# Optimization experiments

Hardware: AMD Instinct MI355X
Metric: run time of the kernel (lower is better)

Reference implementation:

```python
import jax, jax.numpy as jnp
import numpy as np

NEG_SLOPE = 0.2


def gat_layer(x, W, a_src, a_dst, b, src, dst, n_nodes):
    """Single-head GATConv (PyG defaults: heads=1, concat, leaky_relu 0.2, bias)."""
    h = x @ W                                  # [N, hid]
    e_src = h @ a_src                          # [N] per-source logits
    e_dst = h @ a_dst                          # [N] per-dest logits
    e = jax.nn.leaky_relu(e_src[src] + e_dst[dst], NEG_SLOPE)  # [E]
    # numerically-stable softmax over variable-degree dst neighborhoods
    m = jax.ops.segment_max(e, dst, num_segments=n_nodes)
    ex = jnp.exp(e - m[dst])
    s = jax.ops.segment_sum(ex, dst, num_segments=n_nodes)
    alpha = ex / s[dst]                        # [E]
    out = jax.ops.segment_sum(alpha[:, None] * h[src], dst, num_segments=n_nodes)
    return out + b


def setup_inputs() -> dict:
    key = jax.random.key(0)
    N, E, F_IN, HID = 100000, 3200000, 128, 64
    ks = jax.random.split(key, 16)
    x = jax.random.normal(ks[0], (N, F_IN), dtype=jnp.float32)
    edge_index = jax.random.randint(ks[1], (2, E), 0, N, dtype=jnp.int64)
    d = {"x": x, "edge_index": edge_index}
    dims = [(F_IN, HID), (HID, HID), (HID, HID)]
    for i, (din, dout) in enumerate(dims, start=1):
        sc = 1.0 / np.sqrt(din)
        d[f"W{i}"] = jax.random.normal(ks[4 * i], (din, dout), dtype=jnp.float32) * sc
        d[f"a_src{i}"] = jax.random.normal(ks[4 * i + 1], (dout,), dtype=jnp.float32) * 0.1
        d[f"a_dst{i}"] = jax.random.normal(ks[4 * i + 2], (dout,), dtype=jnp.float32) * 0.1
        d[f"b{i}"] = jnp.zeros((dout,), dtype=jnp.float32)
    return d


def reference(x, edge_index, W1, a_src1, a_dst1, b1, W2, a_src2, a_dst2, b2, W3, a_src3, a_dst3, b3):
    n_nodes = x.shape[0]
    loops = jnp.arange(n_nodes, dtype=edge_index.dtype)
    src = jnp.concatenate([edge_index[0], loops])   # add_self_loops=True (PyG default)
    dst = jnp.concatenate([edge_index[1], loops])
    h = jax.nn.relu(gat_layer(x, W1, a_src1, a_dst1, b1, src, dst, n_nodes))
    h = jax.nn.relu(gat_layer(h, W2, a_src2, a_dst2, b2, src, dst, n_nodes))
    h = gat_layer(h, W3, a_src3, a_dst3, b3, src, dst, n_nodes)
    return h
```

## Files before the change

### kernel.cpp

```cpp
#include <hip/hip_runtime.h>
#include <math.h>

#define NEG_SLOPE 0.2f
#define SH 9
#define BINW (1 << SH)
#define TILE 4096

static __device__ __forceinline__ float leaky(float x) { return x > 0.f ? x : NEG_SLOPE * x; }


__global__ void zero_int_kernel(int* __restrict__ p, int n) {
    int i = blockIdx.x * blockDim.x + threadIdx.x;
    if (i < n) p[i] = 0;
}


__global__ __launch_bounds__(256) void histo_bins_kernel(const int* __restrict__ ei_dst, int E,
                                                         int* __restrict__ bin_cnt) {
    __shared__ int hl[256];
    hl[threadIdx.x] = 0;
    __syncthreads();
    int stride = gridDim.x * blockDim.x;
    for (int e = blockIdx.x * blockDim.x + threadIdx.x; e < E; e += stride)
        atomicAdd(&hl[ei_dst[e] >> SH], 1);
    __syncthreads();
    int v = hl[threadIdx.x];
    if (v) atomicAdd(&bin_cnt[threadIdx.x], v);
}

__global__ void scan_bins_kernel(const int* __restrict__ bin_cnt, int nbin,
                                 int* __restrict__ bin_base, int* __restrict__ bin_cur) {
    __shared__ int buf[256];
    int t = threadIdx.x;
    int v = (t < nbin) ? bin_cnt[t] : 0;
    buf[t] = v;
    __syncthreads();
    for (int off = 1; off < 256; off <<= 1) {
        int tv = (t >= off) ? buf[t - off] : 0;
        __syncthreads();
        buf[t] += tv;
        __syncthreads();
    }
    if (t < nbin) {
        int excl = buf[t] - v;
        bin_base[t] = excl;
        bin_cur[t] = excl;
    }
    if (t == nbin - 1) bin_base[nbin] = buf[t];
}

__global__ __launch_bounds__(256) void bin_sort_kernel(const int* __restrict__ ei, int E, int nbin,
                                                       int* __restrict__ bin_cur,
                                                       unsigned* __restrict__ staged) {
    __shared__ unsigned sorted[TILE];
    __shared__ unsigned char binIdx[TILE];
    __shared__ int hist[256];
    __shared__ int binstart[256];
    __shared__ int goff[256];
    int tid = threadIdx.x;
    int tile0 = blockIdx.x * TILE;
    int cnt = min(TILE, E - tile0);
    hist[tid] = 0;
    __syncthreads();
    unsigned mys[16];
    int myb[16], myo[16];
#pragma unroll
    for (int r = 0; r < 16; r++) {
        int idx = tile0 + tid + r * 256;
        if (idx < E) {
            int s = ei[idx], d = ei[E + idx];
            myb[r] = d >> SH;
            mys[r] = ((unsigned)(d & (BINW - 1)) << 17) | (unsigned)s;
            myo[r] = atomicAdd(&hist[myb[r]], 1);
        } else {
            myb[r] = -1;
        }
    }
    __syncthreads();
    int v = hist[tid];
    binstart[tid] = v;
    __syncthreads();
    for (int off = 1; off < 256; off <<= 1) {
        int t = (tid >= off) ? binstart[tid - off] : 0;
        __syncthreads();
        binstart[tid] += t;
        __syncthreads();
    }
    int incl = binstart[tid];
    __syncthreads();
    binstart[tid] = incl - v;
    if (tid < nbin && v > 0) goff[tid] = atomicAdd(&bin_cur[tid], v);
    __syncthreads();
#pragma unroll
    for (int r = 0; r < 16; r++) {
        if (myb[r] >= 0) {
            int lp = binstart[myb[r]] + myo[r];
            sorted[lp] = mys[r];
            binIdx[lp] = (unsigned char)myb[r];
        }
    }
    __syncthreads();
    for (int i = tid; i < cnt; i += 256) {
        int b = binIdx[i];
        staged[goff[b] + (i - binstart[b])] = sorted[i];
    }
}

__global__ __launch_bounds__(512) void bin_finalize_kernel(const unsigned* __restrict__ staged,
                                                           const int* __restrict__ bin_base,
                                                           int N, int* __restrict__ rowptr,
                                                           int* __restrict__ csr_src) {
    __shared__ int deg[BINW];
    __shared__ int scanbuf[BINW];
    int bin = blockIdx.x, t = threadIdx.x;
    int base = bin << SH;
    int nd = min(BINW, N - base);
    int bs = bin_base[bin], be = bin_base[bin + 1];
    deg[t] = 0;
    __syncthreads();
    for (int i = bs + t; i < be; i += 512) atomicAdd(&deg[staged[i] >> 17], 1);
    __syncthreads();
    int v = (t < nd) ? deg[t] : 0;
    scanbuf[t] = v;
    __syncthreads();
    for (int off = 1; off < BINW; off <<= 1) {
        int tv = (t >= off) ? scanbuf[t - off] : 0;
        __syncthreads();
        scanbuf[t] += tv;
        __syncthreads();
    }
    int excl = bs + scanbuf[t] - v;
    if (t < nd) rowptr[base + t] = excl;
    if (t == 0) rowptr[base + nd] = be;
    __syncthreads();
    if (t < nd) deg[t] = excl;
    __syncthreads();
    for (int i = bs + t; i < be; i += 512) {
        unsigned e = staged[i];
        int pos = atomicAdd(&deg[e >> 17], 1);
        csr_src[pos] = (int)(e & 0x1FFFFu);
    }
}


template <int K>
__global__ __launch_bounds__(256) void gemm_logits_kernel(
        const float* __restrict__ x, const float* __restrict__ W,
        const float* __restrict__ a_src, const float* __restrict__ a_dst, int n,
        float* __restrict__ h, float* __restrict__ esrc, float* __restrict__ edst) {
    __shared__ float xs[64 * K];
    const int tid = threadIdx.x;
    const int lane = tid & 63;
    const int wv = tid >> 6;

    float wr[K];
#pragma unroll
    for (int k = 0; k < K; k++) wr[k] = W[k * 64 + lane];
    const float asl = a_src[lane], adl = a_dst[lane];

    const int row0 = blockIdx.x * 64;

    constexpr int F4_PER_ROW = K / 4;
    constexpr int NP = 64 * F4_PER_ROW / 256;
#pragma unroll
    for (int p = 0; p < NP; p++) {
        int f = p * 256 + tid;
        int row = f / F4_PER_ROW;
        int slot = f % F4_PER_ROW;
        int gr = row0 + row;
        if (gr >= n) gr = n - 1;
        *reinterpret_cast<float4*>(&xs[row * K + slot * 4]) =
            *reinterpret_cast<const float4*>(&x[(size_t)gr * K + slot * 4]);
    }
    __syncthreads();

    for (int g2 = 0; g2 < 4; g2++) {
        const int lr = wv * 16 + g2 * 4;
        const float* b0 = &xs[(lr + 0) * K];
        const float* b1 = &xs[(lr + 1) * K];
        const float* b2 = &xs[(lr + 2) * K];
        const float* b3 = &xs[(lr + 3) * K];
        float a0 = 0.f, a1 = 0.f, a2 = 0.f, a3 = 0.f;
#pragma unroll
        for (int q = 0; q < K / 4; q++) {
            float4 f0 = *reinterpret_cast<const float4*>(&b0[q * 4]);
            float4 f1 = *reinterpret_cast<const float4*>(&b1[q * 4]);
            float4 f2 = *reinterpret_cast<const float4*>(&b2[q * 4]);
            float4 f3 = *reinterpret_cast<const float4*>(&b3[q * 4]);
            a0 += f0.x * wr[4 * q + 0] + f0.y * wr[4 * q + 1] + f0.z * wr[4 * q + 2] + f0.w * wr[4 * q + 3];
            a1 += f1.x * wr[4 * q + 0] + f1.y * wr[4 * q + 1] + f1.z * wr[4 * q + 2] + f1.w * wr[4 * q + 3];
            a2 += f2.x * wr[4 * q + 0] + f2.y * wr[4 * q + 1] + f2.z * wr[4 * q + 2] + f2.w * wr[4 * q + 3];
            a3 += f3.x * wr[4 * q + 0] + f3.y * wr[4 * q + 1] + f3.z * wr[4 * q + 2] + f3.w * wr[4 * q + 3];
        }
        float s0 = a0 * asl, d0 = a0 * adl;
        float s1 = a1 * asl, d1 = a1 * adl;
        float s2 = a2 * asl, d2 = a2 * adl;
        float s3 = a3 * asl, d3 = a3 * adl;
#pragma unroll
        for (int o = 32; o; o >>= 1) {
            s0 += __shfl_xor(s0, o); d0 += __shfl_xor(d0, o);
            s1 += __shfl_xor(s1, o); d1 += __shfl_xor(d1, o);
            s2 += __shfl_xor(s2, o); d2 += __shfl_xor(d2, o);
            s3 += __shfl_xor(s3, o); d3 += __shfl_xor(d3, o);
        }
        const int r0 = row0 + lr;
        if (r0 + 0 < n) h[(size_t)(r0 + 0) * 64 + lane] = a0;
        if (r0 + 1 < n) h[(size_t)(r0 + 1) * 64 + lane] = a1;
        if (r0 + 2 < n) h[(size_t)(r0 + 2) * 64 + lane] = a2;
        if (r0 + 3 < n) h[(size_t)(r0 + 3) * 64 + lane] = a3;
        if (lane == 0) {
            if (r0 + 0 < n) { esrc[r0 + 0] = s0; edst[r0 + 0] = d0; }
            if (r0 + 1 < n) { esrc[r0 + 1] = s1; edst[r0 + 1] = d1; }
            if (r0 + 2 < n) { esrc[r0 + 2] = s2; edst[r0 + 2] = d2; }
            if (r0 + 3 < n) { esrc[r0 + 3] = s3; edst[r0 + 3] = d3; }
        }
    }
}


#define GATHER8(J)                                                                  \
    {                                                                               \
        float w0 = __shfl(w, (J) + 0), w1 = __shfl(w, (J) + 1);                     \
        float w2 = __shfl(w, (J) + 2), w3 = __shfl(w, (J) + 3);                     \
        float w4_ = __shfl(w, (J) + 4), w5 = __shfl(w, (J) + 5);                    \
        float w6 = __shfl(w, (J) + 6), w7 = __shfl(w, (J) + 7);                     \
        int s0 = __shfl(sN, (J) + 0), s1 = __shfl(sN, (J) + 1);                     \
        int s2 = __shfl(sN, (J) + 2), s3 = __shfl(sN, (J) + 3);                     \
        int s4 = __shfl(sN, (J) + 4), s5 = __shfl(sN, (J) + 5);                     \
        int s6 = __shfl(sN, (J) + 6), s7 = __shfl(sN, (J) + 7);                     \
        float g0 = h[(size_t)s0 * 64 + lane], g1 = h[(size_t)s1 * 64 + lane];       \
        float g2 = h[(size_t)s2 * 64 + lane], g3 = h[(size_t)s3 * 64 + lane];       \
        float g4 = h[(size_t)s4 * 64 + lane], g5 = h[(size_t)s5 * 64 + lane];       \
        float g6 = h[(size_t)s6 * 64 + lane], g7 = h[(size_t)s7 * 64 + lane];       \
        acc += w0 * g0; acc += w1 * g1; acc += w2 * g2; acc += w3 * g3;             \
        acc += w4_ * g4; acc += w5 * g5; acc += w6 * g6; acc += w7 * g7;            \
    }

__global__ __launch_bounds__(256) void gat_aggregate_kernel(
        const float* __restrict__ h, const float* __restrict__ esrc, const float* __restrict__ edst,
        const int* __restrict__ rowptr, const int* __restrict__ csr_src,
        const float* __restrict__ bias, int n, int do_relu, float* __restrict__ out) {
    int wave = threadIdx.x >> 6, lane = threadIdx.x & 63;
    for (int dst = blockIdx.x * 4 + wave; dst < n; dst += gridDim.x * 4) {
        int rs = rowptr[dst], re = rowptr[dst + 1];
        int deg = re - rs;
        float ed = edst[dst];
        float eself = leaky(esrc[dst] + ed);
        float acc;
        if (deg <= 64) {
            int i = rs + lane;
            bool valid = i < re;
            int sN = valid ? csr_src[i] : 0;
            float e = valid ? leaky(esrc[sN] + ed) : -1e30f;
            float m = fmaxf(e, eself);
#pragma unroll
            for (int off = 32; off; off >>= 1) m = fmaxf(m, __shfl_xor(m, off));
            float p = valid ? expf(e - m) : 0.f;
            float s = p;
#pragma unroll
            for (int off = 32; off; off >>= 1) s += __shfl_xor(s, off);
            float pself = expf(eself - m);
            s += pself;
            float inv_s = 1.f / s;
            acc = pself * inv_s * h[(size_t)dst * 64 + lane];
            float w = p * inv_s;
            int j = 0;
            for (; j + 8 <= deg; j += 8) GATHER8(j);
            for (; j < deg; j++) {
                float wj = __shfl(w, j);
                int sj = __shfl(sN, j);
                acc += wj * h[(size_t)sj * 64 + lane];
            }
        } else {
            float m = eself, s = (lane == 0) ? 1.f : 0.f;
            for (int i = rs + lane; i < re; i += 64) {
                int sN = csr_src[i];
                float e = leaky(esrc[sN] + ed);
                float nm = fmaxf(m, e);
                s = s * expf(m - nm) + expf(e - nm);
                m = nm;
            }
#pragma unroll
            for (int off = 32; off; off >>= 1) {
                float m2 = __shfl_xor(m, off), s2 = __shfl_xor(s, off);
                float nm = fmaxf(m, m2);
                s = s * expf(m - nm) + s2 * expf(m2 - nm);
                m = nm;
            }
            float inv_s = 1.f / s;
            acc = expf(eself - m) * inv_s * h[(size_t)dst * 64 + lane];
            for (int base = rs; base < re; base += 64) {
                int i = base + lane;
                int sN = 0;
                float w = 0.f;
                if (i < re) {
                    sN = csr_src[i];
                    w = expf(leaky(esrc[sN] + ed) - m) * inv_s;
                }
                int cnt = min(64, re - base);
                int j = 0;
                for (; j + 8 <= cnt; j += 8) GATHER8(j);
                for (; j < cnt; j++) {
                    float wj = __shfl(w, j);
                    int sj = __shfl(sN, j);
                    acc += wj * h[(size_t)sj * 64 + lane];
                }
            }
        }
        float v = acc + bias[lane];
        if (do_relu) v = fmaxf(v, 0.f);
        out[(size_t)dst * 64 + lane] = v;
    }
}


extern "C" void kernel_launch(void* const* d_in, const int* in_sizes, int n_in,
                              void* d_out, int out_size, void* d_ws, size_t ws_size,
                              hipStream_t stream) {
    const float* x = (const float*)d_in[0];
    const int* ei = (const int*)d_in[1];
    const float* W1 = (const float*)d_in[2];
    const float* as1 = (const float*)d_in[3];
    const float* ad1 = (const float*)d_in[4];
    const float* b1 = (const float*)d_in[5];
    const float* W2 = (const float*)d_in[6];
    const float* as2 = (const float*)d_in[7];
    const float* ad2 = (const float*)d_in[8];
    const float* b2 = (const float*)d_in[9];
    const float* W3 = (const float*)d_in[10];
    const float* as3 = (const float*)d_in[11];
    const float* ad3 = (const float*)d_in[12];
    const float* b3 = (const float*)d_in[13];

    const int FIN = 128, HID = 64;
    int N = in_sizes[0] / FIN;
    int E = in_sizes[1] / 2;
    int nbin = (N + BINW - 1) >> SH;

    char* base = (char*)d_ws;
    size_t off = 0;
    auto alloc = [&](size_t bytes) -> void* {
        void* p = base + off;
        off = (off + bytes + 255) & ~(size_t)255;
        return p;
    };
    int* rowptr = (int*)alloc((size_t)(N + 1) * 4);
    int* bin_cnt = (int*)alloc((size_t)nbin * 4);
    int* bin_base = (int*)alloc((size_t)(nbin + 1) * 4);
    int* bin_cur = (int*)alloc((size_t)nbin * 4);
    int* csr_src = (int*)alloc((size_t)E * 4);
    float* esrc = (float*)alloc((size_t)N * 4);
    float* edst = (float*)alloc((size_t)N * 4);
    float* hA = (float*)alloc((size_t)N * HID * 4);
    unsigned* staged = (unsigned*)hA;
    (void)ws_size;
    (void)n_in;

    float* out = (float*)d_out;

    zero_int_kernel<<<1, 256, 0, stream>>>(bin_cnt, nbin);
    histo_bins_kernel<<<2048, 256, 0, stream>>>(ei + E, E, bin_cnt);
    scan_bins_kernel<<<1, 256, 0, stream>>>(bin_cnt, nbin, bin_base, bin_cur);
    bin_sort_kernel<<<(E + TILE - 1) / TILE, 256, 0, stream>>>(ei, E, nbin, bin_cur, staged);
    bin_finalize_kernel<<<nbin, 512, 0, stream>>>(staged, bin_base, N, rowptr, csr_src);

    int agrid = (N + 3) / 4;
    int ggrid = (N + 63) / 64;

    gemm_logits_kernel<128><<<ggrid, 256, 0, stream>>>(x, W1, as1, ad1, N, hA, esrc, edst);
    gat_aggregate_kernel<<<agrid, 256, 0, stream>>>(hA, esrc, edst, rowptr, csr_src, b1, N, 1, out);
    gemm_logits_kernel<64><<<ggrid, 256, 0, stream>>>(out, W2, as2, ad2, N, hA, esrc, edst);
    gat_aggregate_kernel<<<agrid, 256, 0, stream>>>(hA, esrc, edst, rowptr, csr_src, b2, N, 1, out);
    gemm_logits_kernel<64><<<ggrid, 256, 0, stream>>>(out, W3, as3, ad3, N, hA, esrc, edst);
    gat_aggregate_kernel<<<agrid, 256, 0, stream>>>(hA, esrc, edst, rowptr, csr_src, b3, N, 0, out);
}
```

Baseline: 675.1 us.

## Gather neighbor rows as float4 with four edges per wave in parallel

The aggregation kernel now splits each 64-lane wave into four 16-lane groups. Each group loads a full 256-byte neighbor row as float4, so four edges are gathered at once instead of one edge per instruction with scalar loads. The partial sums are reduced across the groups with xor shuffles, and only 16 lanes write the float4 output. This cuts the number of load instructions and shuffles per edge, at the cost of an extra cross-lane reduction and some idle lanes in the tail loops.

```diff
diff --git a/kernel.cpp b/kernel.cpp
--- a/kernel.cpp
+++ b/kernel.cpp
@@ -218,35 +218,32 @@
 }
 
 
-#define GATHER8(J)                                                                  \
-    {                                                                               \
-        float w0 = __shfl(w, (J) + 0), w1 = __shfl(w, (J) + 1);                     \
-        float w2 = __shfl(w, (J) + 2), w3 = __shfl(w, (J) + 3);                     \
-        float w4_ = __shfl(w, (J) + 4), w5 = __shfl(w, (J) + 5);                    \
-        float w6 = __shfl(w, (J) + 6), w7 = __shfl(w, (J) + 7);                     \
-        int s0 = __shfl(sN, (J) + 0), s1 = __shfl(sN, (J) + 1);                     \
-        int s2 = __shfl(sN, (J) + 2), s3 = __shfl(sN, (J) + 3);                     \
-        int s4 = __shfl(sN, (J) + 4), s5 = __shfl(sN, (J) + 5);                     \
-        int s6 = __shfl(sN, (J) + 6), s7 = __shfl(sN, (J) + 7);                     \
-        float g0 = h[(size_t)s0 * 64 + lane], g1 = h[(size_t)s1 * 64 + lane];       \
-        float g2 = h[(size_t)s2 * 64 + lane], g3 = h[(size_t)s3 * 64 + lane];       \
-        float g4 = h[(size_t)s4 * 64 + lane], g5 = h[(size_t)s5 * 64 + lane];       \
-        float g6 = h[(size_t)s6 * 64 + lane], g7 = h[(size_t)s7 * 64 + lane];       \
-        acc += w0 * g0; acc += w1 * g1; acc += w2 * g2; acc += w3 * g3;             \
-        acc += w4_ * g4; acc += w5 * g5; acc += w6 * g6; acc += w7 * g7;            \
+#define QUAD2(J)                                                                     \
+    {                                                                                \
+        int j0 = (J) + sub, j1 = (J) + 4 + sub;                                      \
+        float w0 = __shfl(w, j0), w1 = __shfl(w, j1);                                \
+        int s0 = __shfl(sN, j0), s1 = __shfl(sN, j1);                                \
+        float4 g0 = *reinterpret_cast<const float4*>(&h[(size_t)s0 * 64 + c4 * 4]);  \
+        float4 g1 = *reinterpret_cast<const float4*>(&h[(size_t)s1 * 64 + c4 * 4]);  \
+        acc.x += w0 * g0.x; acc.y += w0 * g0.y; acc.z += w0 * g0.z; acc.w += w0 * g0.w; \
+        acc.x += w1 * g1.x; acc.y += w1 * g1.y; acc.z += w1 * g1.z; acc.w += w1 * g1.w; \
     }
 
 __global__ __launch_bounds__(256) void gat_aggregate_kernel(
         const float* __restrict__ h, const float* __restrict__ esrc, const float* __restrict__ edst,
         const int* __restrict__ rowptr, const int* __restrict__ csr_src,
         const float* __restrict__ bias, int n, int do_relu, float* __restrict__ out) {
-    int wave = threadIdx.x >> 6, lane = threadIdx.x & 63;
+    const int wave = threadIdx.x >> 6, lane = threadIdx.x & 63;
+    const int sub = lane >> 4;
+    const int c4 = lane & 15;
+    const float4 bf = *reinterpret_cast<const float4*>(&bias[c4 * 4]);
     for (int dst = blockIdx.x * 4 + wave; dst < n; dst += gridDim.x * 4) {
         int rs = rowptr[dst], re = rowptr[dst + 1];
         int deg = re - rs;
         float ed = edst[dst];
         float eself = leaky(esrc[dst] + ed);
-        float acc;
+        float4 acc = make_float4(0.f, 0.f, 0.f, 0.f);
+        float pselfw;
         if (deg <= 64) {
             int i = rs + lane;
             bool valid = i < re;
@@ -262,14 +259,19 @@
             float pself = expf(eself - m);
             s += pself;
             float inv_s = 1.f / s;
-            acc = pself * inv_s * h[(size_t)dst * 64 + lane];
+            pselfw = pself * inv_s;
             float w = p * inv_s;
             int j = 0;
-            for (; j + 8 <= deg; j += 8) GATHER8(j);
-            for (; j < deg; j++) {
-                float wj = __shfl(w, j);
-                int sj = __shfl(sN, j);
-                acc += wj * h[(size_t)sj * 64 + lane];
+            for (; j + 8 <= deg; j += 8) QUAD2(j);
+            for (; j < deg; j += 4) {
+                int jj = j + sub;
+                int jjc = jj < 63 ? jj : 63;
+                float wj = __shfl(w, jjc);
+                int sj = __shfl(sN, jjc);
+                if (jj < deg) {
+                    float4 g = *reinterpret_cast<const float4*>(&h[(size_t)sj * 64 + c4 * 4]);
+                    acc.x += wj * g.x; acc.y += wj * g.y; acc.z += wj * g.z; acc.w += wj * g.w;
+                }
             }
         } else {
             float m = eself, s = (lane == 0) ? 1.f : 0.f;
@@ -288,28 +290,47 @@
                 m = nm;
             }
             float inv_s = 1.f / s;
-            acc = expf(eself - m) * inv_s * h[(size_t)dst * 64 + lane];
-            for (int base = rs; base < re; base += 64) {
-                int i = base + lane;
+            pselfw = expf(eself - m) * inv_s;
+            for (int base2 = rs; base2 < re; base2 += 64) {
+                int i = base2 + lane;
+                int cnt = min(64, re - base2);
                 int sN = 0;
                 float w = 0.f;
                 if (i < re) {
                     sN = csr_src[i];
                     w = expf(leaky(esrc[sN] + ed) - m) * inv_s;
                 }
-                int cnt = min(64, re - base);
                 int j = 0;
-                for (; j + 8 <= cnt; j += 8) GATHER8(j);
-                for (; j < cnt; j++) {
-                    float wj = __shfl(w, j);
-                    int sj = __shfl(sN, j);
-                    acc += wj * h[(size_t)sj * 64 + lane];
+                for (; j + 8 <= cnt; j += 8) QUAD2(j);
+                for (; j < cnt; j += 4) {
+                    int jj = j + sub;
+                    int jjc = jj < 63 ? jj : 63;
+                    float wj = __shfl(w, jjc);
+                    int sj = __shfl(sN, jjc);
+                    if (jj < cnt) {
+                        float4 g = *reinterpret_cast<const float4*>(&h[(size_t)sj * 64 + c4 * 4]);
+                        acc.x += wj * g.x; acc.y += wj * g.y; acc.z += wj * g.z; acc.w += wj * g.w;
+                    }
                 }
             }
         }
-        float v = acc + bias[lane];
-        if (do_relu) v = fmaxf(v, 0.f);
-        out[(size_t)dst * 64 + lane] = v;
+        if (sub == 0) {
+            float4 gs = *reinterpret_cast<const float4*>(&h[(size_t)dst * 64 + c4 * 4]);
+            acc.x += pselfw * gs.x; acc.y += pselfw * gs.y;
+            acc.z += pselfw * gs.z; acc.w += pselfw * gs.w;
+        }
+        acc.x += __shfl_xor(acc.x, 16); acc.y += __shfl_xor(acc.y, 16);
+        acc.z += __shfl_xor(acc.z, 16); acc.w += __shfl_xor(acc.w, 16);
+        acc.x += __shfl_xor(acc.x, 32); acc.y += __shfl_xor(acc.y, 32);
+        acc.z += __shfl_xor(acc.z, 32); acc.w += __shfl_xor(acc.w, 32);
+        if (lane < 16) {
+            float4 v = make_float4(acc.x + bf.x, acc.y + bf.y, acc.z + bf.z, acc.w + bf.w);
+            if (do_relu) {
+                v.x = fmaxf(v.x, 0.f); v.y = fmaxf(v.y, 0.f);
+                v.z = fmaxf(v.z, 0.f); v.w = fmaxf(v.w, 0.f);
+            }
+            *reinterpret_cast<float4*>(&out[(size_t)dst * 64 + c4 * 4]) = v;
+        }
     }
 }
 
```

After: 684.2 us. Within noise of the previous version (+1.4%).
